# Performance work log

Measured on AMD Instinct MI355X. Metric: run time of the kernel, lower is better.

The kernel has to match this reference:

```python
import jax, jax.numpy as jnp
import numpy as np

B, I, H, O = 16384, 512, 1024, 512

def setup_inputs() -> dict:
    key = jax.random.key(0)
    ks = jax.random.split(key, 8)
    s_x = 1.0 / np.sqrt(I)
    s_h = 1.0 / np.sqrt(H)
    inp = jax.random.normal(ks[0], (B, I), jnp.float32)
    h = jax.random.normal(ks[1], (B, H), jnp.float32)
    c = jax.random.normal(ks[2], (B, H), jnp.float32)
    # stacked gate weights, order [i, o, f, z]
    Wx = jax.random.uniform(ks[3], (4, H, I), jnp.float32, -s_x, s_x)
    Wh = jax.random.uniform(ks[4], (4, H, H), jnp.float32, -s_h, s_h)
    # z-gate h2z weight is re-initialized with standard normal in reset_parameters
    Wh = Wh.at[3].set(jax.random.normal(ks[5], (H, H), jnp.float32))
    # biases per module init: i=linspace(-1,-10), o=0, f=linspace(1,10), z=0
    bx = jnp.stack([
        jnp.linspace(-1.0, -10.0, H, dtype=jnp.float32),
        jnp.zeros((H,), jnp.float32),
        jnp.linspace(1.0, 10.0, H, dtype=jnp.float32),
        jnp.zeros((H,), jnp.float32),
    ])
    Wout = jax.random.uniform(ks[6], (O, H), jnp.float32, -s_h, s_h)
    bout = jax.random.uniform(ks[7], (O,), jnp.float32, -s_h, s_h)
    return {"inp": inp, "h": h, "c": c, "Wx": Wx, "bx": bx, "Wh": Wh,
            "Wout": Wout, "bout": bout}

def reference(inp, h, c, Wx, bx, Wh, Wout, bout):
    # fused gate pre-activations: two stacked GEMMs
    # gx: [4, B, H], gh: [4, B, H]
    gx = jnp.einsum('bi,ghi->gbh', inp, Wx) + bx[:, None, :]
    gh = jnp.einsum('bh,gkh->gbk', h, Wh)
    g = gx + gh
    i = jax.nn.sigmoid(g[0])
    o = jax.nn.sigmoid(g[1])
    f = jax.nn.sigmoid(g[2])
    z = jnp.tanh(g[3])
    c_new = i * z + f * c
    h_new = o * jnp.tanh(c_new)  # act_fn = tanh
    out = h_new @ Wout.T + bout
    return (out, h_new)
```

## Files before the change

### kernel.cpp

```cpp
#include <hip/hip_runtime.h>
#include <stdint.h>

#define BB 16384
#define II 512
#define HH 1024
#define OO 512

typedef short s16x8 __attribute__((ext_vector_type(8)));
typedef float f32x4 __attribute__((ext_vector_type(4)));

__device__ __forceinline__ unsigned short f2bf(float x) {
  union { float f; unsigned u; } v; v.f = x;
  return (unsigned short)((v.u + 0x7fffu + ((v.u >> 16) & 1u)) >> 16);
}
__device__ __forceinline__ float bf2f(unsigned short b) {
  union { unsigned u; float f; } v; v.u = ((unsigned)b) << 16;
  return v.f;
}
__device__ __forceinline__ float sigmoid_f(float x) {
  return 1.0f / (1.0f + __expf(-x));
}
__device__ __forceinline__ float tanh_f(float x) {
  float ax = fabsf(x);
  float e = __expf(-2.0f * ax);
  float t = (1.0f - e) / (1.0f + e);
  return x >= 0.0f ? t : -t;
}

__device__ __forceinline__ void stage16(const void* g, void* l) {
  __builtin_amdgcn_global_load_lds((const __attribute__((address_space(1))) void*)g,
                                   (__attribute__((address_space(3))) void*)l,
                                   16, 0, 0);
}

__device__ __forceinline__ void mma_step64(const unsigned short* As, const unsigned short* Bs,
                                           f32x4 acc[4][4], int lane, int wave) {
  const int wm = wave & 1, wn = wave >> 1;
  const int ln = lane & 15, q = lane >> 4;
#pragma unroll
  for (int s = 0; s < 2; ++s) {
    s16x8 af[4], bfr[4];
#pragma unroll
    for (int i = 0; i < 4; ++i) {
      const int r = wm * 64 + i * 16 + ln;
      af[i] = *(const s16x8*)(As + r * 64 + ((((s << 2) + q) + r) & 7) * 8);
    }
#pragma unroll
    for (int i = 0; i < 4; ++i) {
      const int r = wn * 64 + i * 16 + ln;
      bfr[i] = *(const s16x8*)(Bs + r * 64 + ((((s << 2) + q) + r) & 7) * 8);
    }
#pragma unroll
    for (int mi = 0; mi < 4; ++mi)
#pragma unroll
      for (int ni = 0; ni < 4; ++ni)
        acc[mi][ni] = __builtin_amdgcn_mfma_f32_16x16x32_bf16(af[mi], bfr[ni], acc[mi][ni], 0, 0, 0);
  }
}


__global__ __launch_bounds__(256) void prep_X(const float* __restrict__ inp,
                                              const float* __restrict__ h,
                                              unsigned short* __restrict__ Xb,
                                              unsigned short* __restrict__ Hlo) {
  int t = blockIdx.x * 256 + threadIdx.x;
  int base = t * 8;
  int b = base / 1536;
  int k = base - b * 1536;
  const float* src = (k < 512) ? (inp + b * 512 + k) : (h + b * 1024 + (k - 512));
  float4 v0 = *(const float4*)src;
  float4 v1 = *(const float4*)(src + 4);
  float f[8] = {v0.x, v0.y, v0.z, v0.w, v1.x, v1.y, v1.z, v1.w};
  unsigned short hi[8];
#pragma unroll
  for (int i = 0; i < 8; ++i) hi[i] = f2bf(f[i]);
  *(s16x8*)(Xb + base) = *(s16x8*)hi;
  if (k >= 512) {
    unsigned short lo[8];
#pragma unroll
    for (int i = 0; i < 8; ++i) lo[i] = f2bf(f[i] - bf2f(hi[i]));
    *(s16x8*)(Hlo + b * 1024 + (k - 512)) = *(s16x8*)lo;
  }
}

__global__ __launch_bounds__(256) void prep_Wg(const float* __restrict__ Wx,
                                               const float* __restrict__ Wh,
                                               unsigned short* __restrict__ Wg) {
  int t = blockIdx.x * 256 + threadIdx.x;
  int base = t * 8;
  int n = base / 1536;
  int k = base - n * 1536;
  int r = n & 255;
  int gate = (r >> 4) & 3;
  int unit = ((n >> 8) << 6) + (((r >> 6) & 3) << 4) + (r & 15);
  const float* src = (k < 512) ? (Wx + (gate * 1024 + unit) * 512 + k)
                               : (Wh + (gate * 1024 + unit) * 1024 + (k - 512));
  float4 v0 = *(const float4*)src;
  float4 v1 = *(const float4*)(src + 4);
  float f[8] = {v0.x, v0.y, v0.z, v0.w, v1.x, v1.y, v1.z, v1.w};
  unsigned short o[8];
#pragma unroll
  for (int i = 0; i < 8; ++i) o[i] = f2bf(f[i]);
  *(s16x8*)(Wg + base) = *(s16x8*)o;
}

__global__ __launch_bounds__(256) void prep_Wz2(const float* __restrict__ Whz,
                                                unsigned short* __restrict__ Wz2) {
  int t = blockIdx.x * 256 + threadIdx.x;
  int base = t * 8;
  int n = base >> 11;
  int k = base & 2047;
  int klo = (k < 1024) ? k : (k - 1024);
  const float* src = Whz + n * 1024 + klo;
  float4 v0 = *(const float4*)src;
  float4 v1 = *(const float4*)(src + 4);
  float f[8] = {v0.x, v0.y, v0.z, v0.w, v1.x, v1.y, v1.z, v1.w};
  unsigned short o[8];
  if (k < 1024) {
#pragma unroll
    for (int i = 0; i < 8; ++i) { unsigned short h_ = f2bf(f[i]); o[i] = f2bf(f[i] - bf2f(h_)); }
  } else {
#pragma unroll
    for (int i = 0; i < 8; ++i) o[i] = f2bf(f[i]);
  }
  *(s16x8*)(Wz2 + base) = *(s16x8*)o;
}

__global__ __launch_bounds__(256) void prep_Wout(const float* __restrict__ Wout,
                                                 unsigned short* __restrict__ Wo) {
  int t = blockIdx.x * 256 + threadIdx.x;
  int base = t * 8;
  float4 v0 = *(const float4*)(Wout + base);
  float4 v1 = *(const float4*)(Wout + base + 4);
  float f[8] = {v0.x, v0.y, v0.z, v0.w, v1.x, v1.y, v1.z, v1.w};
  unsigned short o[8];
#pragma unroll
  for (int i = 0; i < 8; ++i) o[i] = f2bf(f[i]);
  *(s16x8*)(Wo + base) = *(s16x8*)o;
}


#define RD_A(CA, MI, KS) (*(const s16x8*)((CA) + ((KS) ? aoff1 : aoff0) + (MI) * 1024))
#define RD_B(CB, NI, KS) (*(const s16x8*)((CB) + ((KS) ? boff1 : boff0) + (NI) * 1024))
#define VM8 asm volatile("s_waitcnt vmcnt(8)" ::: "memory")
#define VM4 asm volatile("s_waitcnt vmcnt(4)" ::: "memory")
#define VM0 asm volatile("s_waitcnt vmcnt(0)" ::: "memory")
#define LGKM0 asm volatile("s_waitcnt lgkmcnt(0)" ::: "memory")
#define SB0 __builtin_amdgcn_sched_barrier(0)
#define BARR __builtin_amdgcn_s_barrier()
#define VMNONE ((void)0)
#define NOST ((void)0)

#define AQ(S, CA, Q) do { \
  S[0] = RD_A(CA, 2 * (Q), 0);  S[1] = RD_A(CA, 2 * (Q) + 1, 0); \
  S[2] = RD_A(CA, 2 * (Q), 1);  S[3] = RD_A(CA, 2 * (Q) + 1, 1); } while (0)
#define BH(BQ, CB, KS) do { \
  BQ[4 * (KS) + 0] = RD_B(CB, 0, KS); BQ[4 * (KS) + 1] = RD_B(CB, 1, KS); \
  BQ[4 * (KS) + 2] = RD_B(CB, 2, KS); BQ[4 * (KS) + 3] = RD_B(CB, 3, KS); } while (0)

#define SA_H0(TT, DB) do { \
  stage16(gA[0][0] + (size_t)(TT) * 64, (DB)); \
  stage16(gA[0][1] + (size_t)(TT) * 64, (DB) + 4096); } while (0)
#define SA_H1(TT, DB) do { \
  stage16(gA[1][0] + (size_t)(TT) * 64, (DB) + 8192); \
  stage16(gA[1][1] + (size_t)(TT) * 64, (DB) + 12288); } while (0)
#define SB_H0(TT, DB) do { \
  stage16(gB[0][0] + (size_t)(TT) * 64, (DB)); \
  stage16(gB[0][1] + (size_t)(TT) * 64, (DB) + 4096); } while (0)
#define SB_H1(TT, DB) do { \
  stage16(gB[1][0] + (size_t)(TT) * 64, (DB) + 8192); \
  stage16(gB[1][1] + (size_t)(TT) * 64, (DB) + 12288); } while (0)
#define ZSA_H0(TT, DB) do { \
  const unsigned short *z0_, *z1_; \
  if ((TT) < 16) { z0_ = gAX[0][0] + (size_t)(TT) * 64; z1_ = gAX[0][1] + (size_t)(TT) * 64; } \
  else { z0_ = gAH[0][0] + (size_t)((TT) - 16) * 64; z1_ = gAH[0][1] + (size_t)((TT) - 16) * 64; } \
  stage16(z0_, (DB)); stage16(z1_, (DB) + 4096); } while (0)
#define ZSA_H1(TT, DB) do { \
  const unsigned short *z2_, *z3_; \
  if ((TT) < 16) { z2_ = gAX[1][0] + (size_t)(TT) * 64; z3_ = gAX[1][1] + (size_t)(TT) * 64; } \
  else { z2_ = gAH[1][0] + (size_t)((TT) - 16) * 64; z3_ = gAH[1][1] + (size_t)((TT) - 16) * 64; } \
  stage16(z2_, (DB) + 8192); stage16(z3_, (DB) + 12288); } while (0)

#define MFMAQ(Q, S) do { \
  __builtin_amdgcn_s_setprio(1); \
  _Pragma("unroll") \
  for (int ni = 0; ni < 4; ++ni) { \
    acc[2 * (Q)    ][ni] = __builtin_amdgcn_mfma_f32_16x16x32_bf16(S[0], bq[ni], acc[2 * (Q)    ][ni], 0, 0, 0); \
    acc[2 * (Q) + 1][ni] = __builtin_amdgcn_mfma_f32_16x16x32_bf16(S[1], bq[ni], acc[2 * (Q) + 1][ni], 0, 0, 0); \
  } \
  _Pragma("unroll") \
  for (int ni = 0; ni < 4; ++ni) { \
    acc[2 * (Q)    ][ni] = __builtin_amdgcn_mfma_f32_16x16x32_bf16(S[2], bq[4 + ni], acc[2 * (Q)    ][ni], 0, 0, 0); \
    acc[2 * (Q) + 1][ni] = __builtin_amdgcn_mfma_f32_16x16x32_bf16(S[3], bq[4 + ni], acc[2 * (Q) + 1][ni], 0, 0, 0); \
  } \
  __builtin_amdgcn_s_setprio(0); \
} while (0)

#define KTILE(CA, CB, S0, S1, S2, S3, VMX) do { \
  s16x8 bq[8], aE[4], aO[4]; \
  BH(bq, CB, 0); BH(bq, CB, 1); \
  AQ(aE, CA, 0); \
  S0; \
  BARR; LGKM0; SB0; \
  MFMAQ(0, aE); \
  AQ(aO, CA, 1); S1; \
  BARR; LGKM0; SB0; \
  MFMAQ(1, aO); \
  AQ(aE, CA, 2); S2; \
  BARR; LGKM0; SB0; \
  MFMAQ(2, aE); \
  AQ(aO, CA, 3); S3; \
  BARR; LGKM0; SB0; \
  MFMAQ(3, aO); \
  VMX; BARR; \
} while (0)

__global__ __launch_bounds__(512, 2) void gemm_gates2(const unsigned short* __restrict__ Xb,
                                                      const unsigned short* __restrict__ Wg,
                                                      const float* __restrict__ bx,
                                                      const float* __restrict__ cold,
                                                      const unsigned short* __restrict__ Dgz,
                                                      float* __restrict__ hnew,
                                                      unsigned short* __restrict__ hnewb) {
  __shared__ unsigned short lds[2][2][16384];
  const int tid = threadIdx.x;
  const int lane = tid & 63, wave = tid >> 6;
  const int wm = wave & 1, wn = wave >> 1;
  const int ln = lane & 15, qlane = lane >> 4;
  const int n0 = blockIdx.x << 8, m0 = blockIdx.y << 8;
  const int sr = tid >> 3;
  const int j = ((tid & 7) - (sr & 7)) & 7;

  const unsigned short* gA[2][2];
  const unsigned short* gB[2][2];
#pragma unroll
  for (int hh = 0; hh < 2; ++hh)
#pragma unroll
    for (int u = 0; u < 2; ++u) {
      const int row = hh * 128 + u * 64 + sr;
      gA[hh][u] = Xb + (size_t)(m0 + row) * 1536 + j * 8;
      gB[hh][u] = Wg + (size_t)(n0 + row) * 1536 + j * 8;
    }
  unsigned short* const dA0 = &lds[0][0][0] + (tid & ~63) * 8;
  unsigned short* const dB0 = &lds[0][1][0] + (tid & ~63) * 8;
  unsigned short* const dA1 = &lds[1][0][0] + (tid & ~63) * 8;
  unsigned short* const dB1 = &lds[1][1][0] + (tid & ~63) * 8;
  const unsigned short* const lA0 = &lds[0][0][0];
  const unsigned short* const lB0 = &lds[0][1][0];
  const unsigned short* const lA1 = &lds[1][0][0];
  const unsigned short* const lB1 = &lds[1][1][0];
  const int sl0 = ((qlane + ln) & 7) * 8;
  const int sl1 = sl0 ^ 32;
  const int aoff0 = (wm * 128 + ln) * 64 + sl0;
  const int aoff1 = (wm * 128 + ln) * 64 + sl1;
  const int boff0 = (wn * 64 + ln) * 64 + sl0;
  const int boff1 = (wn * 64 + ln) * 64 + sl1;

  f32x4 acc[8][4] = {};

  SA_H0(0, dA0); SA_H1(0, dA0); SB_H0(0, dB0); SB_H1(0, dB0);
  SA_H0(1, dA1); SA_H1(1, dA1); SB_H0(1, dB1); SB_H1(1, dB1);
  VM8;
  BARR;

  KTILE(lA0, lB0, NOST, NOST, SB_H0(2, dB0), SB_H1(2, dB0), VM4);
#pragma unroll 1
  for (int t = 1; t < 21; t += 2) {
    KTILE(lA1, lB1, SA_H0(t + 1, dA0), SA_H1(t + 1, dA0),
                    SB_H0(t + 2, dB1), SB_H1(t + 2, dB1), VM4);
    KTILE(lA0, lB0, SA_H0(t + 2, dA1), SA_H1(t + 2, dA1),
                    SB_H0(t + 3, dB0), SB_H1(t + 3, dB0), VM4);
  }
  KTILE(lA1, lB1, SA_H0(22, dA0), SA_H1(22, dA0),
                  SB_H0(23, dB1), SB_H1(23, dB1), VM4);
  KTILE(lA0, lB0, SA_H0(23, dA1), SA_H1(23, dA1), NOST, NOST, VM0);
  KTILE(lA1, lB1, NOST, NOST, NOST, NOST, VMNONE);

  const int unit = ((int)blockIdx.x << 6) + (wn << 4) + ln;
  const float bi = bx[unit];
  const float bo = bx[1024 + unit];
  const float bfg = bx[2048 + unit];
  const float bz = bx[3072 + unit];
#pragma unroll
  for (int mi = 0; mi < 8; ++mi) {
#pragma unroll
    for (int r = 0; r < 4; ++r) {
      const int b = m0 + wm * 128 + mi * 16 + qlane * 4 + r;
      const int idx = b * 1024 + unit;
      const float gi = acc[mi][0][r] + bi;
      const float go = acc[mi][1][r] + bo;
      const float gf = acc[mi][2][r] + bfg;
      const float gz = acc[mi][3][r] + bz + bf2f(Dgz[idx]);
      const float iv = sigmoid_f(gi);
      const float ov = sigmoid_f(go);
      const float fv = sigmoid_f(gf);
      const float zv = tanh_f(gz);
      const float cn = iv * zv + fv * cold[idx];
      const float hn = ov * tanh_f(cn);
      hnew[idx] = hn;
      hnewb[idx] = f2bf(hn);
    }
  }
}

__global__ __launch_bounds__(512, 2) void gemm_zcorr2(const unsigned short* __restrict__ Xb,
                                                      const unsigned short* __restrict__ Hlo,
                                                      const unsigned short* __restrict__ Wz2,
                                                      unsigned short* __restrict__ Dgz) {
  __shared__ unsigned short lds[2][2][16384];
  const int tid = threadIdx.x;
  const int lane = tid & 63, wave = tid >> 6;
  const int wm = wave & 1, wn = wave >> 1;
  const int ln = lane & 15, qlane = lane >> 4;
  const int n0 = blockIdx.x << 8, m0 = blockIdx.y << 8;
  const int sr = tid >> 3;
  const int j = ((tid & 7) - (sr & 7)) & 7;

  const unsigned short* gAX[2][2];
  const unsigned short* gAH[2][2];
  const unsigned short* gB[2][2];
#pragma unroll
  for (int hh = 0; hh < 2; ++hh)
#pragma unroll
    for (int u = 0; u < 2; ++u) {
      const int row = hh * 128 + u * 64 + sr;
      gAX[hh][u] = Xb  + (size_t)(m0 + row) * 1536 + 512 + j * 8;
      gAH[hh][u] = Hlo + (size_t)(m0 + row) * 1024 + j * 8;
      gB[hh][u]  = Wz2 + (size_t)(n0 + row) * 2048 + j * 8;
    }
  unsigned short* const dA0 = &lds[0][0][0] + (tid & ~63) * 8;
  unsigned short* const dB0 = &lds[0][1][0] + (tid & ~63) * 8;
  unsigned short* const dA1 = &lds[1][0][0] + (tid & ~63) * 8;
  unsigned short* const dB1 = &lds[1][1][0] + (tid & ~63) * 8;
  const unsigned short* const lA0 = &lds[0][0][0];
  const unsigned short* const lB0 = &lds[0][1][0];
  const unsigned short* const lA1 = &lds[1][0][0];
  const unsigned short* const lB1 = &lds[1][1][0];
  const int sl0 = ((qlane + ln) & 7) * 8;
  const int sl1 = sl0 ^ 32;
  const int aoff0 = (wm * 128 + ln) * 64 + sl0;
  const int aoff1 = (wm * 128 + ln) * 64 + sl1;
  const int boff0 = (wn * 64 + ln) * 64 + sl0;
  const int boff1 = (wn * 64 + ln) * 64 + sl1;

  f32x4 acc[8][4] = {};

  ZSA_H0(0, dA0); ZSA_H1(0, dA0); SB_H0(0, dB0); SB_H1(0, dB0);
  ZSA_H0(1, dA1); ZSA_H1(1, dA1); SB_H0(1, dB1); SB_H1(1, dB1);
  VM8;
  BARR;

  KTILE(lA0, lB0, NOST, NOST, SB_H0(2, dB0), SB_H1(2, dB0), VM4);
#pragma unroll 1
  for (int t = 1; t < 29; t += 2) {
    KTILE(lA1, lB1, ZSA_H0(t + 1, dA0), ZSA_H1(t + 1, dA0),
                    SB_H0(t + 2, dB1), SB_H1(t + 2, dB1), VM4);
    KTILE(lA0, lB0, ZSA_H0(t + 2, dA1), ZSA_H1(t + 2, dA1),
                    SB_H0(t + 3, dB0), SB_H1(t + 3, dB0), VM4);
  }
  KTILE(lA1, lB1, ZSA_H0(30, dA0), ZSA_H1(30, dA0),
                  SB_H0(31, dB1), SB_H1(31, dB1), VM4);
  KTILE(lA0, lB0, ZSA_H0(31, dA1), ZSA_H1(31, dA1), NOST, NOST, VM0);
  KTILE(lA1, lB1, NOST, NOST, NOST, NOST, VMNONE);

#pragma unroll
  for (int mi = 0; mi < 8; ++mi) {
#pragma unroll
    for (int r = 0; r < 4; ++r) {
      const int b = m0 + wm * 128 + mi * 16 + qlane * 4 + r;
#pragma unroll
      for (int ni = 0; ni < 4; ++ni) {
        const int n = n0 + wn * 64 + ni * 16 + ln;
        Dgz[b * 1024 + n] = f2bf(acc[mi][ni][r]);
      }
    }
  }
}

__global__ __launch_bounds__(256) void gemm_out(const unsigned short* __restrict__ Hb,
                                                const unsigned short* __restrict__ Wo,
                                                const float* __restrict__ bout,
                                                float* __restrict__ out) {
  __shared__ unsigned short As[8192];
  __shared__ unsigned short Bs[8192];
  const int n0 = blockIdx.x * 128;
  const int m0 = blockIdx.y * 128;
  const int tid = threadIdx.x, lane = tid & 63, wave = tid >> 6;
  const unsigned short *ga[4], *gb[4];
  unsigned short *la[4], *lb[4];
#pragma unroll
  for (int u = 0; u < 4; ++u) {
    int p = u * 256 + tid;
    int r = p >> 3;
    int jj = ((p & 7) - r) & 7;
    ga[u] = Hb + (size_t)(m0 + r) * 1024 + jj * 8;
    gb[u] = Wo + (size_t)(n0 + r) * 1024 + jj * 8;
    la[u] = As + (u * 256 + (tid & ~63)) * 8;
    lb[u] = Bs + (u * 256 + (tid & ~63)) * 8;
  }
  f32x4 acc[4][4] = {};
  for (int kk = 0; kk < 16; ++kk) {
#pragma unroll
    for (int u = 0; u < 4; ++u) { stage16(ga[u], la[u]); stage16(gb[u], lb[u]); }
#pragma unroll
    for (int u = 0; u < 4; ++u) { ga[u] += 64; gb[u] += 64; }
    __syncthreads();
    mma_step64(As, Bs, acc, lane, wave);
    __syncthreads();
  }
  const int wm = wave & 1, wn = wave >> 1;
  const int ln = lane & 15, q = lane >> 4;
  float bo_[4];
#pragma unroll
  for (int ni = 0; ni < 4; ++ni) bo_[ni] = bout[n0 + wn * 64 + ni * 16 + ln];
#pragma unroll
  for (int mi = 0; mi < 4; ++mi) {
#pragma unroll
    for (int r = 0; r < 4; ++r) {
      const int b = m0 + wm * 64 + mi * 16 + q * 4 + r;
#pragma unroll
      for (int ni = 0; ni < 4; ++ni) {
        const int n = n0 + wn * 64 + ni * 16 + ln;
        out[b * 512 + n] = acc[mi][ni][r] + bo_[ni];
      }
    }
  }
}

extern "C" void kernel_launch(void* const* d_in, const int* in_sizes, int n_in,
                              void* d_out, int out_size, void* d_ws, size_t ws_size,
                              hipStream_t stream) {
  const float* inp  = (const float*)d_in[0];
  const float* h    = (const float*)d_in[1];
  const float* c    = (const float*)d_in[2];
  const float* Wx   = (const float*)d_in[3];
  const float* bx   = (const float*)d_in[4];
  const float* Wh   = (const float*)d_in[5];
  const float* Wout = (const float*)d_in[6];
  const float* bout = (const float*)d_in[7];

  float* out  = (float*)d_out;
  float* hnew = out + (size_t)BB * OO;

  char* ws = (char*)d_ws;
  unsigned short* Xb  = (unsigned short*)(ws);
  unsigned short* Wg  = (unsigned short*)(ws + 50331648);
  unsigned short* Wo  = (unsigned short*)(ws + 62914560);
  unsigned short* Hb  = (unsigned short*)(ws + 63963136);
  unsigned short* Hlo = (unsigned short*)(ws + 97517568);
  unsigned short* Wz2 = (unsigned short*)(ws + 131072000);
  unsigned short* Dgz = (unsigned short*)(ws + 135266304);

  prep_X   <<<12288, 256, 0, stream>>>(inp, h, Xb, Hlo);
  prep_Wg  <<<3072,  256, 0, stream>>>(Wx, Wh, Wg);
  prep_Wz2 <<<1024,  256, 0, stream>>>(Wh + 3 * 1024 * 1024, Wz2);
  prep_Wout<<<256,   256, 0, stream>>>(Wout, Wo);
  gemm_zcorr2<<<dim3(4, 64),  512, 0, stream>>>(Xb, Hlo, Wz2, Dgz);
  gemm_gates2<<<dim3(16, 64), 512, 0, stream>>>(Xb, Wg, bx, c, Dgz, hnew, Hb);
  gemm_out  <<<dim3(4, 128),  256, 0, stream>>>(Hb, Wo, bout, out);
}
```

Baseline: 558.6 us.

## Merge prep kernels into one launch and add extra barriers in GEMM k-tile

The four fp32-to-bf16 prep kernels are merged into a single kernel that dispatches on block index, removing three launches and the gaps between them. Inside the gates GEMM k-tile, a partial LDS wait (lgkmcnt(8)) is placed before the first barrier and an extra workgroup barrier is added after each MFMA quarter. The barriers appear aimed at keeping waves in lockstep so LDS reads and global staging interleave with MFMA work, but they add synchronisation points to the hot loop.

```diff
diff --git a/kernel.cpp b/kernel.cpp
--- a/kernel.cpp
+++ b/kernel.cpp
@@ -58,85 +58,84 @@
   }
 }
 
-
-__global__ __launch_bounds__(256) void prep_X(const float* __restrict__ inp,
-                                              const float* __restrict__ h,
-                                              unsigned short* __restrict__ Xb,
-                                              unsigned short* __restrict__ Hlo) {
-  int t = blockIdx.x * 256 + threadIdx.x;
-  int base = t * 8;
-  int b = base / 1536;
-  int k = base - b * 1536;
-  const float* src = (k < 512) ? (inp + b * 512 + k) : (h + b * 1024 + (k - 512));
-  float4 v0 = *(const float4*)src;
-  float4 v1 = *(const float4*)(src + 4);
-  float f[8] = {v0.x, v0.y, v0.z, v0.w, v1.x, v1.y, v1.z, v1.w};
-  unsigned short hi[8];
-#pragma unroll
-  for (int i = 0; i < 8; ++i) hi[i] = f2bf(f[i]);
-  *(s16x8*)(Xb + base) = *(s16x8*)hi;
-  if (k >= 512) {
-    unsigned short lo[8];
-#pragma unroll
-    for (int i = 0; i < 8; ++i) lo[i] = f2bf(f[i] - bf2f(hi[i]));
-    *(s16x8*)(Hlo + b * 1024 + (k - 512)) = *(s16x8*)lo;
-  }
-}
-
-__global__ __launch_bounds__(256) void prep_Wg(const float* __restrict__ Wx,
-                                               const float* __restrict__ Wh,
-                                               unsigned short* __restrict__ Wg) {
-  int t = blockIdx.x * 256 + threadIdx.x;
-  int base = t * 8;
-  int n = base / 1536;
-  int k = base - n * 1536;
-  int r = n & 255;
-  int gate = (r >> 4) & 3;
-  int unit = ((n >> 8) << 6) + (((r >> 6) & 3) << 4) + (r & 15);
-  const float* src = (k < 512) ? (Wx + (gate * 1024 + unit) * 512 + k)
-                               : (Wh + (gate * 1024 + unit) * 1024 + (k - 512));
-  float4 v0 = *(const float4*)src;
-  float4 v1 = *(const float4*)(src + 4);
-  float f[8] = {v0.x, v0.y, v0.z, v0.w, v1.x, v1.y, v1.z, v1.w};
-  unsigned short o[8];
-#pragma unroll
-  for (int i = 0; i < 8; ++i) o[i] = f2bf(f[i]);
-  *(s16x8*)(Wg + base) = *(s16x8*)o;
-}
-
-__global__ __launch_bounds__(256) void prep_Wz2(const float* __restrict__ Whz,
-                                                unsigned short* __restrict__ Wz2) {
-  int t = blockIdx.x * 256 + threadIdx.x;
-  int base = t * 8;
-  int n = base >> 11;
-  int k = base & 2047;
-  int klo = (k < 1024) ? k : (k - 1024);
-  const float* src = Whz + n * 1024 + klo;
-  float4 v0 = *(const float4*)src;
-  float4 v1 = *(const float4*)(src + 4);
-  float f[8] = {v0.x, v0.y, v0.z, v0.w, v1.x, v1.y, v1.z, v1.w};
-  unsigned short o[8];
-  if (k < 1024) {
-#pragma unroll
-    for (int i = 0; i < 8; ++i) { unsigned short h_ = f2bf(f[i]); o[i] = f2bf(f[i] - bf2f(h_)); }
+__global__ __launch_bounds__(256) void prep_all(const float* __restrict__ inp,
+                                                const float* __restrict__ h,
+                                                const float* __restrict__ Wx,
+                                                const float* __restrict__ Wh,
+                                                const float* __restrict__ Wout,
+                                                unsigned short* __restrict__ Xb,
+                                                unsigned short* __restrict__ Hlo,
+                                                unsigned short* __restrict__ Wg,
+                                                unsigned short* __restrict__ Wz2,
+                                                unsigned short* __restrict__ Wo) {
+  const int bid = blockIdx.x;
+  if (bid < 12288) {
+    int t = bid * 256 + threadIdx.x;
+    int base = t * 8;
+    int b = base / 1536;
+    int k = base - b * 1536;
+    const float* src = (k < 512) ? (inp + b * 512 + k) : (h + b * 1024 + (k - 512));
+    float4 v0 = *(const float4*)src;
+    float4 v1 = *(const float4*)(src + 4);
+    float f[8] = {v0.x, v0.y, v0.z, v0.w, v1.x, v1.y, v1.z, v1.w};
+    unsigned short hi[8];
+#pragma unroll
+    for (int i = 0; i < 8; ++i) hi[i] = f2bf(f[i]);
+    *(s16x8*)(Xb + base) = *(s16x8*)hi;
+    if (k >= 512) {
+      unsigned short lo[8];
+#pragma unroll
+      for (int i = 0; i < 8; ++i) lo[i] = f2bf(f[i] - bf2f(hi[i]));
+      *(s16x8*)(Hlo + b * 1024 + (k - 512)) = *(s16x8*)lo;
+    }
+  } else if (bid < 15360) {
+    int t = (bid - 12288) * 256 + threadIdx.x;
+    int base = t * 8;
+    int n = base / 1536;
+    int k = base - n * 1536;
+    int r = n & 255;
+    int gate = (r >> 4) & 3;
+    int unit = ((n >> 8) << 6) + (((r >> 6) & 3) << 4) + (r & 15);
+    const float* src = (k < 512) ? (Wx + (gate * 1024 + unit) * 512 + k)
+                                 : (Wh + (gate * 1024 + unit) * 1024 + (k - 512));
+    float4 v0 = *(const float4*)src;
+    float4 v1 = *(const float4*)(src + 4);
+    float f[8] = {v0.x, v0.y, v0.z, v0.w, v1.x, v1.y, v1.z, v1.w};
+    unsigned short o[8];
+#pragma unroll
+    for (int i = 0; i < 8; ++i) o[i] = f2bf(f[i]);
+    *(s16x8*)(Wg + base) = *(s16x8*)o;
+  } else if (bid < 16384) {
+    const float* Whz = Wh + 3 * 1024 * 1024;
+    int t = (bid - 15360) * 256 + threadIdx.x;
+    int base = t * 8;
+    int n = base >> 11;
+    int k = base & 2047;
+    int klo = (k < 1024) ? k : (k - 1024);
+    const float* src = Whz + n * 1024 + klo;
+    float4 v0 = *(const float4*)src;
+    float4 v1 = *(const float4*)(src + 4);
+    float f[8] = {v0.x, v0.y, v0.z, v0.w, v1.x, v1.y, v1.z, v1.w};
+    unsigned short o[8];
+    if (k < 1024) {
+#pragma unroll
+      for (int i = 0; i < 8; ++i) { unsigned short h_ = f2bf(f[i]); o[i] = f2bf(f[i] - bf2f(h_)); }
+    } else {
+#pragma unroll
+      for (int i = 0; i < 8; ++i) o[i] = f2bf(f[i]);
+    }
+    *(s16x8*)(Wz2 + base) = *(s16x8*)o;
   } else {
+    int t = (bid - 16384) * 256 + threadIdx.x;
+    int base = t * 8;
+    float4 v0 = *(const float4*)(Wout + base);
+    float4 v1 = *(const float4*)(Wout + base + 4);
+    float f[8] = {v0.x, v0.y, v0.z, v0.w, v1.x, v1.y, v1.z, v1.w};
+    unsigned short o[8];
 #pragma unroll
     for (int i = 0; i < 8; ++i) o[i] = f2bf(f[i]);
-  }
-  *(s16x8*)(Wz2 + base) = *(s16x8*)o;
-}
-
-__global__ __launch_bounds__(256) void prep_Wout(const float* __restrict__ Wout,
-                                                 unsigned short* __restrict__ Wo) {
-  int t = blockIdx.x * 256 + threadIdx.x;
-  int base = t * 8;
-  float4 v0 = *(const float4*)(Wout + base);
-  float4 v1 = *(const float4*)(Wout + base + 4);
-  float f[8] = {v0.x, v0.y, v0.z, v0.w, v1.x, v1.y, v1.z, v1.w};
-  unsigned short o[8];
-#pragma unroll
-  for (int i = 0; i < 8; ++i) o[i] = f2bf(f[i]);
-  *(s16x8*)(Wo + base) = *(s16x8*)o;
+    *(s16x8*)(Wo + base) = *(s16x8*)o;
+  }
 }
 
 
@@ -145,6 +144,7 @@
 #define VM8 asm volatile("s_waitcnt vmcnt(8)" ::: "memory")
 #define VM4 asm volatile("s_waitcnt vmcnt(4)" ::: "memory")
 #define VM0 asm volatile("s_waitcnt vmcnt(0)" ::: "memory")
+#define LGKM8 asm volatile("s_waitcnt lgkmcnt(8)" ::: "memory")
 #define LGKM0 asm volatile("s_waitcnt lgkmcnt(0)" ::: "memory")
 #define SB0 __builtin_amdgcn_sched_barrier(0)
 #define BARR __builtin_amdgcn_s_barrier()
@@ -201,14 +201,18 @@
   BH(bq, CB, 0); BH(bq, CB, 1); \
   AQ(aE, CA, 0); \
   S0; \
+  LGKM8; \
   BARR; LGKM0; SB0; \
   MFMAQ(0, aE); \
+  BARR; \
   AQ(aO, CA, 1); S1; \
   BARR; LGKM0; SB0; \
   MFMAQ(1, aO); \
+  BARR; \
   AQ(aE, CA, 2); S2; \
   BARR; LGKM0; SB0; \
   MFMAQ(2, aE); \
+  BARR; \
   AQ(aO, CA, 3); S3; \
   BARR; LGKM0; SB0; \
   MFMAQ(3, aO); \
@@ -451,10 +455,7 @@
   unsigned short* Wz2 = (unsigned short*)(ws + 131072000);
   unsigned short* Dgz = (unsigned short*)(ws + 135266304);
 
-  prep_X   <<<12288, 256, 0, stream>>>(inp, h, Xb, Hlo);
-  prep_Wg  <<<3072,  256, 0, stream>>>(Wx, Wh, Wg);
-  prep_Wz2 <<<1024,  256, 0, stream>>>(Wh + 3 * 1024 * 1024, Wz2);
-  prep_Wout<<<256,   256, 0, stream>>>(Wout, Wo);
+  prep_all<<<16640, 256, 0, stream>>>(inp, h, Wx, Wh, Wout, Xb, Hlo, Wg, Wz2, Wo);
   gemm_zcorr2<<<dim3(4, 64),  512, 0, stream>>>(Xb, Hlo, Wz2, Dgz);
   gemm_gates2<<<dim3(16, 64), 512, 0, stream>>>(Xb, Wg, bx, c, Dgz, hnew, Hb);
   gemm_out  <<<dim3(4, 128),  256, 0, stream>>>(Hb, Wo, bout, out);
```

Result: no change. 551.8 us (-1.2%).
